# Kernel tuning notes

Hardware: AMD Instinct MI355X
Metric: run time of the kernel (lower is better)

## Reference

```python
import jax, jax.numpy as jnp
import numpy as np

N, F, B, D = 1500000, 64, 256, 64
S = B * D

def _lin(x, w, b):
    return x @ w + b

def setup_inputs() -> dict:
    key = jax.random.key(0)
    ks = jax.random.split(key, 32)
    def w(k, i, o):
        return jax.random.normal(k, (i, o), dtype=jnp.float32) * (1.0 / np.sqrt(i))
    inp = {
        "x": jax.random.normal(ks[0], (N, F), dtype=jnp.float32),
        "segment_ids": jnp.sort(jax.random.randint(ks[1], (N,), 0, S)),
        "B": B, "D": D,
        # table_forward (used inside no_grad kernel_forward)
        "tfc0_w": w(ks[2], F, 128), "tfc0_b": jnp.zeros((128,), jnp.float32),
        "tfc1_w": w(ks[3], 128, 32), "tfc1_b": jnp.zeros((32,), jnp.float32),
        # three kernel heads
        "fwd0_w": w(ks[4], 32, 64), "fwd0_b": jnp.zeros((64,), jnp.float32),
        "fwd1_w": w(ks[5], 64, 1), "fwd1_b": jnp.zeros((1,), jnp.float32),
        "com0_w": w(ks[6], 32, 64), "com0_b": jnp.zeros((64,), jnp.float32),
        "com1_w": w(ks[7], 64, 1), "com1_b": jnp.zeros((1,), jnp.float32),
        "bwd0_w": w(ks[8], 32, 64), "bwd0_b": jnp.zeros((64,), jnp.float32),
        "bwd1_w": w(ks[9], 64, 1), "bwd1_b": jnp.zeros((1,), jnp.float32),
        # rl table stack
        "rl0_w": w(ks[10], F, 128), "rl0_b": jnp.zeros((128,), jnp.float32),
        "rl1_w": w(ks[11], 128, 32), "rl1_b": jnp.zeros((32,), jnp.float32),
        # cost MLP
        "cost0_w": w(ks[12], 3, 64), "cost0_b": jnp.zeros((64,), jnp.float32),
        "cost1_w": w(ks[13], 64, 32), "cost1_b": jnp.zeros((32,), jnp.float32),
        # policy net
        "pol_w": w(ks[14], 64, 1), "pol_b": jnp.zeros((1,), jnp.float32),
    }
    return inp

def reference(x, segment_ids, B, D,
              tfc0_w, tfc0_b, tfc1_w, tfc1_b,
              fwd0_w, fwd0_b, fwd1_w, fwd1_b,
              com0_w, com0_b, com1_w, com1_b,
              bwd0_w, bwd0_b, bwd1_w, bwd1_b,
              rl0_w, rl0_b, rl1_w, rl1_b,
              cost0_w, cost0_b, cost1_w, cost1_b,
              pol_w, pol_b):
    S_ = B * D
    # kernel_forward (run under torch.no_grad in original)
    h = jax.nn.relu(_lin(x, tfc0_w, tfc0_b))        # [N,128]
    h = jax.nn.relu(_lin(h, tfc1_w, tfc1_b))        # [N,32]
    seg = jax.ops.segment_sum(h, segment_ids, num_segments=S_)  # [S,32]
    def head(w0, b0, w1, b1):
        return _lin(jax.nn.relu(_lin(seg, w0, b0)), w1, b1).ravel()  # [S]
    fwd_c = head(fwd0_w, fwd0_b, fwd1_w, fwd1_b)
    com_c = head(com0_w, com0_b, com1_w, com1_b)
    bwd_c = head(bwd0_w, bwd0_b, bwd1_w, bwd1_b)
    # _get_latent concatenates in kernel_forward return order (fwd, comm, bwd)
    cost_obs = jax.lax.stop_gradient(
        jnp.stack([fwd_c, com_c, bwd_c], axis=-1)).reshape(B, D, 3)
    c = jax.nn.relu(_lin(cost_obs, cost0_w, cost0_b))
    c = jax.nn.relu(_lin(c, cost1_w, cost1_b))       # [B,D,32]
    # rl table branch (differentiable)
    r = jax.nn.relu(_lin(x, rl0_w, rl0_b))
    r = jax.nn.relu(_lin(r, rl1_w, rl1_b))           # [N,32]
    r = jax.ops.segment_sum(r, segment_ids, num_segments=S_).reshape(B, D, 32)
    latent = jnp.concatenate([r, c], axis=-1)        # [B,D,64]
    logits = _lin(latent, pol_w, pol_b).squeeze(-1)  # [B,D]
    return logits
```

## Files before the change

kernel.cpp:

```cpp
#include <hip/hip_runtime.h>

typedef unsigned short u16;
typedef __bf16  bf16x8 __attribute__((ext_vector_type(8)));
typedef float   f32x4  __attribute__((ext_vector_type(4)));

#define N_ROWS 1500000
#define S_SEG  16384
#define ROWS_PB 32
#define TILES_PB 15
#define GRID_MAIN 3125

#define XS_LD  72
#define H1B_LD 264
#define H2B_LD 66

__device__ __forceinline__ u16 f2bf(float f) {
    union { __bf16 h; u16 u; } cv;
    cv.h = (__bf16)f;
    return cv.u;
}

__global__ void zero_ws_kernel(float* p, int n4) {
    int i = blockIdx.x * 256 + threadIdx.x;
    if (i < n4) reinterpret_cast<float4*>(p)[i] = make_float4(0.f, 0.f, 0.f, 0.f);
}

__global__ void transpose_weights(const float* __restrict__ w0, const float* __restrict__ w1,
                                  const float* __restrict__ r0, const float* __restrict__ r1,
                                  u16* __restrict__ w0T, u16* __restrict__ w1T,
                                  u16* __restrict__ r0T, u16* __restrict__ r1T) {
    int idx = blockIdx.x * 256 + threadIdx.x;
    if (idx < 8192) {
        int o = idx >> 6, k = idx & 63;
        w0T[o * 64 + k] = f2bf(w0[k * 128 + o]);
    } else if (idx < 12288) {
        int t = idx - 8192; int o = t >> 7, k = t & 127;
        w1T[o * 128 + k] = f2bf(w1[k * 32 + o]);
    } else if (idx < 20480) {
        int t = idx - 12288; int o = t >> 6, k = t & 63;
        r0T[o * 64 + k] = f2bf(r0[k * 128 + o]);
    } else if (idx < 24576) {
        int t = idx - 20480; int o = t >> 7, k = t & 127;
        r1T[o * 128 + k] = f2bf(r1[k * 32 + o]);
    }
}

__global__ __launch_bounds__(256, 4) void main_mlp_seg(
    const float* __restrict__ x, const int* __restrict__ seg_ids,
    const u16* __restrict__ w0T, const float* __restrict__ b0a,
    const u16* __restrict__ w1T, const float* __restrict__ b1a,
    const u16* __restrict__ r0T, const float* __restrict__ rb0,
    const u16* __restrict__ r1T, const float* __restrict__ rb1,
    float* __restrict__ seg_out, float* __restrict__ rseg_out)
{
    __shared__ u16   xs [2][ROWS_PB * XS_LD];
    __shared__ u16   h1s[ROWS_PB * H1B_LD];
    __shared__ float h2s[ROWS_PB * H2B_LD];
    __shared__ int   s_ids[2][ROWS_PB];
    __shared__ float sred[256];

    const int tid  = threadIdx.x;
    const int wid  = tid >> 6, lane = tid & 63;
    const int m = lane & 15, q = lane >> 4;
    const size_t row0 = (size_t)blockIdx.x * (TILES_PB * ROWS_PB);

    bf16x8 wA[2][2][2];
    float  bz0[2][2];
    #pragma unroll
    for (int br = 0; br < 2; ++br) {
        const u16*   W0 = br ? r0T : w0T;
        const float* B0 = br ? rb0 : b0a;
        #pragma unroll
        for (int ct = 0; ct < 2; ++ct) {
            int n0 = (2 * wid + ct) * 16;
            #pragma unroll
            for (int ks = 0; ks < 2; ++ks)
                wA[br][ct][ks] = *reinterpret_cast<const bf16x8*>(W0 + (n0 + m) * 64 + ks * 32 + q * 8);
            bz0[br][ct] = B0[n0 + m];
        }
    }
    const int brw = wid >> 1, rtw = wid & 1;
    const u16*   W1 = brw ? r1T : w1T;
    const float* B1 = brw ? rb1 : b1a;
    bf16x8 wB[2][4];
    float  bz1[2];
    #pragma unroll
    for (int ct = 0; ct < 2; ++ct) {
        #pragma unroll
        for (int ks = 0; ks < 4; ++ks)
            wB[ct][ks] = *reinterpret_cast<const bf16x8*>(W1 + (ct * 16 + m) * 128 + ks * 32 + q * 8);
        bz1[ct] = B1[ct * 16 + m];
    }

    const int sr = tid >> 4, sc4 = tid & 15;
    const float* xb = x + (row0 + sr) * 64 + sc4 * 4;

    {
        float4 v0 = *reinterpret_cast<const float4*>(xb);
        float4 v1 = *reinterpret_cast<const float4*>(xb + 1024);
        ushort4 p0, p1;
        p0.x = f2bf(v0.x); p0.y = f2bf(v0.y); p0.z = f2bf(v0.z); p0.w = f2bf(v0.w);
        p1.x = f2bf(v1.x); p1.y = f2bf(v1.y); p1.z = f2bf(v1.z); p1.w = f2bf(v1.w);
        *reinterpret_cast<ushort4*>(&xs[0][sr * XS_LD + sc4 * 4]) = p0;
        *reinterpret_cast<ushort4*>(&xs[0][(sr + 16) * XS_LD + sc4 * 4]) = p1;
        if (tid < ROWS_PB) s_ids[0][tid] = seg_ids[row0 + tid];
    }
    float4 xr0 = *reinterpret_cast<const float4*>(xb + 2048);
    float4 xr1 = *reinterpret_cast<const float4*>(xb + 2048 + 1024);
    int idr = 0;
    if (tid < ROWS_PB) idr = seg_ids[row0 + ROWS_PB + tid];
    __syncthreads();

    int cur = 0;
    #pragma unroll 1
    for (int t = 0; t < TILES_PB; ++t) {
        if (t + 1 < TILES_PB) {
            ushort4 p0, p1;
            p0.x = f2bf(xr0.x); p0.y = f2bf(xr0.y); p0.z = f2bf(xr0.z); p0.w = f2bf(xr0.w);
            p1.x = f2bf(xr1.x); p1.y = f2bf(xr1.y); p1.z = f2bf(xr1.z); p1.w = f2bf(xr1.w);
            *reinterpret_cast<ushort4*>(&xs[cur ^ 1][sr * XS_LD + sc4 * 4]) = p0;
            *reinterpret_cast<ushort4*>(&xs[cur ^ 1][(sr + 16) * XS_LD + sc4 * 4]) = p1;
            if (tid < ROWS_PB) s_ids[cur ^ 1][tid] = idr;
        }
        if (t + 2 < TILES_PB) {
            const float* px = xb + (size_t)(t + 2) * 2048;
            xr0 = *reinterpret_cast<const float4*>(px);
            xr1 = *reinterpret_cast<const float4*>(px + 1024);
            if (tid < ROWS_PB) idr = seg_ids[row0 + (size_t)(t + 2) * ROWS_PB + tid];
        }
        #pragma unroll
        for (int rt = 0; rt < 2; ++rt) {
            bf16x8 a0 = *reinterpret_cast<const bf16x8*>(&xs[cur][(rt * 16 + m) * XS_LD + q * 8]);
            bf16x8 a1 = *reinterpret_cast<const bf16x8*>(&xs[cur][(rt * 16 + m) * XS_LD + 32 + q * 8]);
            #pragma unroll
            for (int br = 0; br < 2; ++br) {
                #pragma unroll
                for (int ct = 0; ct < 2; ++ct) {
                    float b = bz0[br][ct];
                    f32x4 acc = {b, b, b, b};
                    acc = __builtin_amdgcn_mfma_f32_16x16x32_bf16(a0, wA[br][ct][0], acc, 0, 0, 0);
                    acc = __builtin_amdgcn_mfma_f32_16x16x32_bf16(a1, wA[br][ct][1], acc, 0, 0, 0);
                    int colg = br * 128 + (2 * wid + ct) * 16 + m;
                    #pragma unroll
                    for (int i = 0; i < 4; ++i)
                        h1s[(rt * 16 + q * 4 + i) * H1B_LD + colg] = f2bf(fmaxf(acc[i], 0.f));
                }
            }
        }
        __syncthreads();

        {
            bf16x8 a[4];
            #pragma unroll
            for (int ks = 0; ks < 4; ++ks)
                a[ks] = *reinterpret_cast<const bf16x8*>(
                    &h1s[(rtw * 16 + m) * H1B_LD + brw * 128 + ks * 32 + q * 8]);
            #pragma unroll
            for (int ct = 0; ct < 2; ++ct) {
                float b = bz1[ct];
                f32x4 acc = {b, b, b, b};
                #pragma unroll
                for (int ks = 0; ks < 4; ++ks)
                    acc = __builtin_amdgcn_mfma_f32_16x16x32_bf16(a[ks], wB[ct][ks], acc, 0, 0, 0);
                int colg = brw * 32 + ct * 16 + m;
                #pragma unroll
                for (int i = 0; i < 4; ++i)
                    h2s[(rtw * 16 + q * 4 + i) * H2B_LD + colg] = fmaxf(acc[i], 0.f);
            }
        }
        __syncthreads();

        {
            int c = tid & 63, g = tid >> 6;
            float* sp  = (c < 32) ? seg_out : rseg_out;
            int    col = c & 31;
            const int* ids = s_ids[cur];
            if (ids[0] == ids[ROWS_PB - 1]) {
                float a = 0.f;
                #pragma unroll
                for (int r = 0; r < 8; ++r)
                    a += h2s[(g * 8 + r) * H2B_LD + c];
                sred[g * 64 + c] = a;
                __syncthreads();
                if (g == 0) {
                    float tt = sred[c] + sred[64 + c] + sred[128 + c] + sred[192 + c];
                    atomicAdd(&sp[ids[0] * 32 + col], tt);
                }
            } else {
                int curid = -1; float acc = 0.f;
                #pragma unroll
                for (int r = 0; r < 8; ++r) {
                    int rr = g * 8 + r;
                    int id = ids[rr];
                    if (id != curid) {
                        if (curid >= 0) atomicAdd(&sp[curid * 32 + col], acc);
                        curid = id; acc = 0.f;
                    }
                    acc += h2s[rr * H2B_LD + c];
                }
                if (curid >= 0) atomicAdd(&sp[curid * 32 + col], acc);
            }
        }
        __syncthreads();
        cur ^= 1;
    }
}

__global__ __launch_bounds__(256) void heads_kernel(
    const float* __restrict__ seg, const float* __restrict__ rseg,
    const float* __restrict__ fwd0_w, const float* __restrict__ fwd0_b,
    const float* __restrict__ fwd1_w, const float* __restrict__ fwd1_b,
    const float* __restrict__ com0_w, const float* __restrict__ com0_b,
    const float* __restrict__ com1_w, const float* __restrict__ com1_b,
    const float* __restrict__ bwd0_w, const float* __restrict__ bwd0_b,
    const float* __restrict__ bwd1_w, const float* __restrict__ bwd1_b,
    const float* __restrict__ cost0_w, const float* __restrict__ cost0_b,
    const float* __restrict__ cost1_w, const float* __restrict__ cost1_b,
    const float* __restrict__ pol_w, const float* __restrict__ pol_b,
    float* __restrict__ out)
{
    __shared__ float s_seg[4][32];
    __shared__ float s_rseg[4][32];
    __shared__ float s_c0[4][64];
    const int tid = threadIdx.x, wid = tid >> 6, lane = tid & 63;
    const int s = blockIdx.x * 4 + wid;

    if (lane < 32) {
        s_seg[wid][lane]  = seg[s * 32 + lane];
        s_rseg[wid][lane] = rseg[s * 32 + lane];
    }
    __syncthreads();

    const float* w0s[3] = {fwd0_w, com0_w, bwd0_w};
    const float* b0s[3] = {fwd0_b, com0_b, bwd0_b};
    const float* w1s[3] = {fwd1_w, com1_w, bwd1_w};
    const float* b1s[3] = {fwd1_b, com1_b, bwd1_b};
    float costs[3];
    #pragma unroll
    for (int hh = 0; hh < 3; ++hh) {
        float t = 0.f;
        #pragma unroll
        for (int k = 0; k < 32; ++k)
            t = fmaf(s_seg[wid][k], w0s[hh][k * 64 + lane], t);
        t = fmaxf(t + b0s[hh][lane], 0.f);
        float red = t * w1s[hh][lane];
        red += __shfl_down(red, 32);
        red += __shfl_down(red, 16);
        red += __shfl_down(red, 8);
        red += __shfl_down(red, 4);
        red += __shfl_down(red, 2);
        red += __shfl_down(red, 1);
        costs[hh] = __shfl(red, 0) + b1s[hh][0];
    }

    float c0 = costs[0] * cost0_w[lane] +
               costs[1] * cost0_w[64 + lane] +
               costs[2] * cost0_w[128 + lane] + cost0_b[lane];
    c0 = fmaxf(c0, 0.f);
    s_c0[wid][lane] = c0;
    __syncthreads();

    int kk = lane & 31;
    float c1 = 0.f;
    #pragma unroll 8
    for (int j = 0; j < 64; ++j)
        c1 = fmaf(s_c0[wid][j], cost1_w[j * 32 + kk], c1);
    c1 = fmaxf(c1 + cost1_b[kk], 0.f);

    float p = 0.f;
    if (lane < 32)
        p = s_rseg[wid][lane] * pol_w[lane] + c1 * pol_w[32 + lane];
    p += __shfl_down(p, 32);
    p += __shfl_down(p, 16);
    p += __shfl_down(p, 8);
    p += __shfl_down(p, 4);
    p += __shfl_down(p, 2);
    p += __shfl_down(p, 1);
    if (lane == 0) out[s] = p + pol_b[0];
}

extern "C" void kernel_launch(void* const* d_in, const int* in_sizes, int n_in,
                              void* d_out, int out_size, void* d_ws, size_t ws_size,
                              hipStream_t stream) {
    const float* x       = (const float*)d_in[0];
    const int*   seg_ids = (const int*)d_in[1];
    const float* tfc0_w = (const float*)d_in[4];
    const float* tfc0_b = (const float*)d_in[5];
    const float* tfc1_w = (const float*)d_in[6];
    const float* tfc1_b = (const float*)d_in[7];
    const float* fwd0_w = (const float*)d_in[8];
    const float* fwd0_b = (const float*)d_in[9];
    const float* fwd1_w = (const float*)d_in[10];
    const float* fwd1_b = (const float*)d_in[11];
    const float* com0_w = (const float*)d_in[12];
    const float* com0_b = (const float*)d_in[13];
    const float* com1_w = (const float*)d_in[14];
    const float* com1_b = (const float*)d_in[15];
    const float* bwd0_w = (const float*)d_in[16];
    const float* bwd0_b = (const float*)d_in[17];
    const float* bwd1_w = (const float*)d_in[18];
    const float* bwd1_b = (const float*)d_in[19];
    const float* rl0_w  = (const float*)d_in[20];
    const float* rl0_b  = (const float*)d_in[21];
    const float* rl1_w  = (const float*)d_in[22];
    const float* rl1_b  = (const float*)d_in[23];
    const float* cost0_w = (const float*)d_in[24];
    const float* cost0_b = (const float*)d_in[25];
    const float* cost1_w = (const float*)d_in[26];
    const float* cost1_b = (const float*)d_in[27];
    const float* pol_w   = (const float*)d_in[28];
    const float* pol_b   = (const float*)d_in[29];

    char* ws = (char*)d_ws;
    const size_t seg_bytes = (size_t)S_SEG * 32 * sizeof(float);
    float* seg  = (float*)ws;
    float* rseg = (float*)(ws + seg_bytes);
    u16* w0T = (u16*)(ws + 2 * seg_bytes);
    u16* w1T = w0T + 128 * 64;
    u16* r0T = w1T + 32 * 128;
    u16* r1T = r0T + 128 * 64;

    int n4 = (int)(2 * seg_bytes / 16);
    zero_ws_kernel<<<(n4 + 255) / 256, 256, 0, stream>>>(seg, n4);
    transpose_weights<<<96, 256, 0, stream>>>(tfc0_w, tfc1_w, rl0_w, rl1_w,
                                              w0T, w1T, r0T, r1T);
    main_mlp_seg<<<GRID_MAIN, 256, 0, stream>>>(
        x, seg_ids, w0T, tfc0_b, w1T, tfc1_b, r0T, rl0_b, r1T, rl1_b, seg, rseg);
    heads_kernel<<<S_SEG / 4, 256, 0, stream>>>(
        seg, rseg,
        fwd0_w, fwd0_b, fwd1_w, fwd1_b,
        com0_w, com0_b, com1_w, com1_b,
        bwd0_w, bwd0_b, bwd1_w, bwd1_b,
        cost0_w, cost0_b, cost1_w, cost1_b,
        pol_w, pol_b, (float*)d_out);
}
```

Measured before the change: 693.5 us.

## Fuse segment reduction into MFMA registers, swizzle LDS, and carry partial sums across tiles

The second-layer results are no longer written to an h2s LDS buffer and reduced in a separate phase. Segment boundaries come from a ballot mask, and each wave reduces its MFMA accumulators directly with cross-lane shuffles. Partial sums for a segment are carried across tiles, so an atomic is issued only when the segment id changes. Other changes: an XOR swizzle on the LDS layouts, operand-swapped layer-1 MFMAs so the h1 store becomes a packed ushort4, and barriers that wait only on LDS rather than draining global loads. Removing a barrier and the shared-memory round trip shortens each tile. The costs are more complex per-wave control flow and shuffle reductions in every segment loop.

```diff
diff --git a/kernel.cpp b/kernel.cpp
--- a/kernel.cpp
+++ b/kernel.cpp
@@ -1,6 +1,7 @@
 #include <hip/hip_runtime.h>
 
 typedef unsigned short u16;
+typedef unsigned long long u64;
 typedef __bf16  bf16x8 __attribute__((ext_vector_type(8)));
 typedef float   f32x4  __attribute__((ext_vector_type(4)));
 
@@ -12,12 +13,16 @@
 
 #define XS_LD  72
 #define H1B_LD 264
-#define H2B_LD 66
 
 __device__ __forceinline__ u16 f2bf(float f) {
     union { __bf16 h; u16 u; } cv;
     cv.h = (__bf16)f;
     return cv.u;
+}
+
+__device__ __forceinline__ void barrier_nodrain() {
+    asm volatile("s_waitcnt lgkmcnt(0)" ::: "memory");
+    __builtin_amdgcn_s_barrier();
 }
 
 __global__ void zero_ws_kernel(float* p, int n4) {
@@ -53,19 +58,18 @@
     const u16* __restrict__ r1T, const float* __restrict__ rb1,
     float* __restrict__ seg_out, float* __restrict__ rseg_out)
 {
-    __shared__ u16   xs [2][ROWS_PB * XS_LD];
-    __shared__ u16   h1s[ROWS_PB * H1B_LD];
-    __shared__ float h2s[ROWS_PB * H2B_LD];
-    __shared__ int   s_ids[2][ROWS_PB];
-    __shared__ float sred[256];
+    __shared__ u16 xs [2][ROWS_PB * XS_LD];
+    __shared__ u16 h1s[ROWS_PB * H1B_LD];
+    __shared__ int s_ids[2][ROWS_PB];
 
     const int tid  = threadIdx.x;
     const int wid  = tid >> 6, lane = tid & 63;
     const int m = lane & 15, q = lane >> 4;
+    const int swm = (m & 7) << 3;
     const size_t row0 = (size_t)blockIdx.x * (TILES_PB * ROWS_PB);
 
     bf16x8 wA[2][2][2];
-    float  bz0[2][2];
+    f32x4  bias0v[2][2];
     #pragma unroll
     for (int br = 0; br < 2; ++br) {
         const u16*   W0 = br ? r0T : w0T;
@@ -76,7 +80,7 @@
             #pragma unroll
             for (int ks = 0; ks < 2; ++ks)
                 wA[br][ct][ks] = *reinterpret_cast<const bf16x8*>(W0 + (n0 + m) * 64 + ks * 32 + q * 8);
-            bz0[br][ct] = B0[n0 + m];
+            bias0v[br][ct] = *reinterpret_cast<const f32x4*>(B0 + n0 + q * 4);
         }
     }
     const int brw = wid >> 1, rtw = wid & 1;
@@ -91,8 +95,19 @@
             wB[ct][ks] = *reinterpret_cast<const bf16x8*>(W1 + (ct * 16 + m) * 128 + ks * 32 + q * 8);
         bz1[ct] = B1[ct * 16 + m];
     }
+    asm volatile("" :
+        "+v"(wA[0][0][0]), "+v"(wA[0][0][1]), "+v"(wA[0][1][0]), "+v"(wA[0][1][1]),
+        "+v"(wA[1][0][0]), "+v"(wA[1][0][1]), "+v"(wA[1][1][0]), "+v"(wA[1][1][1]));
+    asm volatile("" :
+        "+v"(wB[0][0]), "+v"(wB[0][1]), "+v"(wB[0][2]), "+v"(wB[0][3]),
+        "+v"(wB[1][0]), "+v"(wB[1][1]), "+v"(wB[1][2]), "+v"(wB[1][3]));
+    asm volatile("" :
+        "+v"(bias0v[0][0]), "+v"(bias0v[0][1]), "+v"(bias0v[1][0]), "+v"(bias0v[1][1]));
 
     const int sr = tid >> 4, sc4 = tid & 15;
+    const int sws = (sr & 7) << 3;
+    const int xw0 = sr * XS_LD        + ((sc4 * 4) ^ sws);
+    const int xw1 = (sr + 16) * XS_LD + ((sc4 * 4) ^ sws);
     const float* xb = x + (row0 + sr) * 64 + sc4 * 4;
 
     {
@@ -101,26 +116,32 @@
         ushort4 p0, p1;
         p0.x = f2bf(v0.x); p0.y = f2bf(v0.y); p0.z = f2bf(v0.z); p0.w = f2bf(v0.w);
         p1.x = f2bf(v1.x); p1.y = f2bf(v1.y); p1.z = f2bf(v1.z); p1.w = f2bf(v1.w);
-        *reinterpret_cast<ushort4*>(&xs[0][sr * XS_LD + sc4 * 4]) = p0;
-        *reinterpret_cast<ushort4*>(&xs[0][(sr + 16) * XS_LD + sc4 * 4]) = p1;
+        *reinterpret_cast<ushort4*>(&xs[0][xw0]) = p0;
+        *reinterpret_cast<ushort4*>(&xs[0][xw1]) = p1;
         if (tid < ROWS_PB) s_ids[0][tid] = seg_ids[row0 + tid];
     }
     float4 xr0 = *reinterpret_cast<const float4*>(xb + 2048);
     float4 xr1 = *reinterpret_cast<const float4*>(xb + 2048 + 1024);
     int idr = 0;
     if (tid < ROWS_PB) idr = seg_ids[row0 + ROWS_PB + tid];
-    __syncthreads();
+    barrier_nodrain();
+
+    int   pid = -1;
+    float p0a = 0.f, p1a = 0.f;
+    bool  have = false;
+    float* __restrict__ sp = brw ? rseg_out : seg_out;
 
     int cur = 0;
     #pragma unroll 1
     for (int t = 0; t < TILES_PB; ++t) {
+        const int nxt = cur ^ 1;
         if (t + 1 < TILES_PB) {
-            ushort4 p0, p1;
-            p0.x = f2bf(xr0.x); p0.y = f2bf(xr0.y); p0.z = f2bf(xr0.z); p0.w = f2bf(xr0.w);
-            p1.x = f2bf(xr1.x); p1.y = f2bf(xr1.y); p1.z = f2bf(xr1.z); p1.w = f2bf(xr1.w);
-            *reinterpret_cast<ushort4*>(&xs[cur ^ 1][sr * XS_LD + sc4 * 4]) = p0;
-            *reinterpret_cast<ushort4*>(&xs[cur ^ 1][(sr + 16) * XS_LD + sc4 * 4]) = p1;
-            if (tid < ROWS_PB) s_ids[cur ^ 1][tid] = idr;
+            ushort4 pk0, pk1;
+            pk0.x = f2bf(xr0.x); pk0.y = f2bf(xr0.y); pk0.z = f2bf(xr0.z); pk0.w = f2bf(xr0.w);
+            pk1.x = f2bf(xr1.x); pk1.y = f2bf(xr1.y); pk1.z = f2bf(xr1.z); pk1.w = f2bf(xr1.w);
+            *reinterpret_cast<ushort4*>(&xs[nxt][xw0]) = pk0;
+            *reinterpret_cast<ushort4*>(&xs[nxt][xw1]) = pk1;
+            if (tid < ROWS_PB) s_ids[nxt][tid] = idr;
         }
         if (t + 2 < TILES_PB) {
             const float* px = xb + (size_t)(t + 2) * 2048;
@@ -130,79 +151,84 @@
         }
         #pragma unroll
         for (int rt = 0; rt < 2; ++rt) {
-            bf16x8 a0 = *reinterpret_cast<const bf16x8*>(&xs[cur][(rt * 16 + m) * XS_LD + q * 8]);
-            bf16x8 a1 = *reinterpret_cast<const bf16x8*>(&xs[cur][(rt * 16 + m) * XS_LD + 32 + q * 8]);
+            bf16x8 a0 = *reinterpret_cast<const bf16x8*>(
+                &xs[cur][(rt * 16 + m) * XS_LD + ((q * 8) ^ swm)]);
+            bf16x8 a1 = *reinterpret_cast<const bf16x8*>(
+                &xs[cur][(rt * 16 + m) * XS_LD + ((32 + q * 8) ^ swm)]);
             #pragma unroll
             for (int br = 0; br < 2; ++br) {
                 #pragma unroll
                 for (int ct = 0; ct < 2; ++ct) {
-                    float b = bz0[br][ct];
-                    f32x4 acc = {b, b, b, b};
-                    acc = __builtin_amdgcn_mfma_f32_16x16x32_bf16(a0, wA[br][ct][0], acc, 0, 0, 0);
-                    acc = __builtin_amdgcn_mfma_f32_16x16x32_bf16(a1, wA[br][ct][1], acc, 0, 0, 0);
-                    int colg = br * 128 + (2 * wid + ct) * 16 + m;
-                    #pragma unroll
-                    for (int i = 0; i < 4; ++i)
-                        h1s[(rt * 16 + q * 4 + i) * H1B_LD + colg] = f2bf(fmaxf(acc[i], 0.f));
+                    f32x4 acc = bias0v[br][ct];
+                    acc = __builtin_amdgcn_mfma_f32_16x16x32_bf16(wA[br][ct][0], a0, acc, 0, 0, 0);
+                    acc = __builtin_amdgcn_mfma_f32_16x16x32_bf16(wA[br][ct][1], a1, acc, 0, 0, 0);
+                    ushort4 pk;
+                    pk.x = f2bf(fmaxf(acc[0], 0.f));
+                    pk.y = f2bf(fmaxf(acc[1], 0.f));
+                    pk.z = f2bf(fmaxf(acc[2], 0.f));
+                    pk.w = f2bf(fmaxf(acc[3], 0.f));
+                    int col = br * 128 + (2 * wid + ct) * 16 + q * 4;
+                    *reinterpret_cast<ushort4*>(
+                        &h1s[(rt * 16 + m) * H1B_LD + (col ^ swm)]) = pk;
                 }
             }
         }
-        __syncthreads();
+        barrier_nodrain();
 
         {
+            const int* ids = s_ids[cur];
+            int l31 = (lane < 32) ? lane : 0;
+            int ida = ids[l31];
+            int idb = ids[(l31 > 0) ? (l31 - 1) : 0];
+            u64 bmask = __ballot(lane > 0 && lane < 32 && ida != idb);
+
             bf16x8 a[4];
             #pragma unroll
             for (int ks = 0; ks < 4; ++ks)
                 a[ks] = *reinterpret_cast<const bf16x8*>(
-                    &h1s[(rtw * 16 + m) * H1B_LD + brw * 128 + ks * 32 + q * 8]);
+                    &h1s[(rtw * 16 + m) * H1B_LD + ((brw * 128 + ks * 32 + q * 8) ^ swm)]);
+            f32x4 acc0 = {bz1[0], bz1[0], bz1[0], bz1[0]};
+            f32x4 acc1 = {bz1[1], bz1[1], bz1[1], bz1[1]};
             #pragma unroll
-            for (int ct = 0; ct < 2; ++ct) {
-                float b = bz1[ct];
-                f32x4 acc = {b, b, b, b};
+            for (int ks = 0; ks < 4; ++ks) {
+                acc0 = __builtin_amdgcn_mfma_f32_16x16x32_bf16(a[ks], wB[0][ks], acc0, 0, 0, 0);
+                acc1 = __builtin_amdgcn_mfma_f32_16x16x32_bf16(a[ks], wB[1][ks], acc1, 0, 0, 0);
+            }
+
+            int start = 0;
+            while (start < 32) {
+                u64 above = bmask & (~0ull << (start + 1));
+                int end = above ? (int)__builtin_ctzll(above) : 32;
+                int sid = ids[start];
+                if (sid != pid) {
+                    if (have && q == 0) {
+                        atomicAdd(&sp[pid * 32 + m],      p0a);
+                        atomicAdd(&sp[pid * 32 + 16 + m], p1a);
+                    }
+                    pid = sid; p0a = 0.f; p1a = 0.f; have = false;
+                }
+                float s0 = 0.f, s1 = 0.f;
                 #pragma unroll
-                for (int ks = 0; ks < 4; ++ks)
-                    acc = __builtin_amdgcn_mfma_f32_16x16x32_bf16(a[ks], wB[ct][ks], acc, 0, 0, 0);
-                int colg = brw * 32 + ct * 16 + m;
-                #pragma unroll
-                for (int i = 0; i < 4; ++i)
-                    h2s[(rtw * 16 + q * 4 + i) * H2B_LD + colg] = fmaxf(acc[i], 0.f);
+                for (int i = 0; i < 4; ++i) {
+                    int row = rtw * 16 + q * 4 + i;
+                    bool in = (row >= start) && (row < end);
+                    s0 += in ? fmaxf(acc0[i], 0.f) : 0.f;
+                    s1 += in ? fmaxf(acc1[i], 0.f) : 0.f;
+                }
+                s0 += __shfl_xor(s0, 16); s0 += __shfl_xor(s0, 32);
+                s1 += __shfl_xor(s1, 16); s1 += __shfl_xor(s1, 32);
+                if (end > rtw * 16 && start < rtw * 16 + 16) {
+                    p0a += s0; p1a += s1; have = true;
+                }
+                start = end;
             }
         }
-        __syncthreads();
-
-        {
-            int c = tid & 63, g = tid >> 6;
-            float* sp  = (c < 32) ? seg_out : rseg_out;
-            int    col = c & 31;
-            const int* ids = s_ids[cur];
-            if (ids[0] == ids[ROWS_PB - 1]) {
-                float a = 0.f;
-                #pragma unroll
-                for (int r = 0; r < 8; ++r)
-                    a += h2s[(g * 8 + r) * H2B_LD + c];
-                sred[g * 64 + c] = a;
-                __syncthreads();
-                if (g == 0) {
-                    float tt = sred[c] + sred[64 + c] + sred[128 + c] + sred[192 + c];
-                    atomicAdd(&sp[ids[0] * 32 + col], tt);
-                }
-            } else {
-                int curid = -1; float acc = 0.f;
-                #pragma unroll
-                for (int r = 0; r < 8; ++r) {
-                    int rr = g * 8 + r;
-                    int id = ids[rr];
-                    if (id != curid) {
-                        if (curid >= 0) atomicAdd(&sp[curid * 32 + col], acc);
-                        curid = id; acc = 0.f;
-                    }
-                    acc += h2s[rr * H2B_LD + c];
-                }
-                if (curid >= 0) atomicAdd(&sp[curid * 32 + col], acc);
-            }
-        }
-        __syncthreads();
-        cur ^= 1;
+        barrier_nodrain();
+        cur = nxt;
+    }
+    if (have && q == 0) {
+        atomicAdd(&sp[pid * 32 + m],      p0a);
+        atomicAdd(&sp[pid * 32 + 16 + m], p1a);
     }
 }
 
```

New measurement: 815.4 us. +17.6%, slower.
